# Kernel tuning notes

Hardware: AMD Instinct MI355X
Metric: run time of the kernel (lower is better)

## Reference

```python
import jax, jax.numpy as jnp
import numpy as np

N = 50000      # nodes
E = 800000     # edges (avg degree 16)
D_IN = 256
H = 128
D_OUT = 64
L = 3
EPS = 1e-5


def setup_inputs() -> dict:
    key = jax.random.key(0)
    ks = jax.random.split(key, 12)
    s = 0.05
    x = jax.random.normal(ks[0], (N, D_IN), jnp.float32)
    edge_index = jax.random.randint(ks[1], (2, E), 0, N, dtype=jnp.int32)
    edge_attr = jax.random.normal(ks[2], (E,), jnp.float32)
    # in / out projections
    W_in = jax.random.normal(ks[3], (D_IN, H), jnp.float32) * s
    b_in = jnp.zeros((H,), jnp.float32)
    W_out = jax.random.normal(ks[4], (H, D_OUT), jnp.float32) * s
    # per-layer ResGatedGraphConv params (stacked over L layers)
    Wk = jax.random.normal(ks[5], (L, H, H), jnp.float32) * s
    Wq = jax.random.normal(ks[6], (L, H, H), jnp.float32) * s
    Wv = jax.random.normal(ks[7], (L, H, H), jnp.float32) * s
    Ws = jax.random.normal(ks[8], (L, H, H), jnp.float32) * s  # lin_skip (no bias)
    We = jax.random.normal(ks[9], (L, 1, H), jnp.float32) * s  # lin_edge
    bk = jnp.zeros((L, H), jnp.float32)
    bq = jnp.zeros((L, H), jnp.float32)
    bv = jnp.zeros((L, H), jnp.float32)
    be = jnp.zeros((L, H), jnp.float32)
    b_gcn = jnp.zeros((L, H), jnp.float32)  # conv bias
    gamma = jnp.ones((L, H), jnp.float32)
    beta = jnp.zeros((L, H), jnp.float32)
    return {
        "x": x, "edge_attr": edge_attr,
        "W_in": W_in, "b_in": b_in,
        "Wk": Wk, "bk": bk, "Wq": Wq, "bq": bq, "Wv": Wv, "bv": bv,
        "We": We, "be": be, "Ws": Ws, "b_gcn": b_gcn,
        "gamma": gamma, "beta": beta, "W_out": W_out,
        "edge_index": edge_index,
    }


def _layernorm(h, g, b):
    mu = jnp.mean(h, axis=-1, keepdims=True)
    var = jnp.mean((h - mu) ** 2, axis=-1, keepdims=True)
    return (h - mu) * jax.lax.rsqrt(var + EPS) * g + b


def reference(x, edge_attr, W_in, b_in, Wk, bk, Wq, bq, Wv, bv, We, be, Ws,
              b_gcn, gamma, beta, W_out, edge_index):
    src = edge_index[0]  # x_j (source)
    dst = edge_index[1]  # x_i (target)
    ea = edge_attr[:, None]  # [E, 1]
    h = x @ W_in + b_in  # dropout_prob = 0 -> identity
    for l in range(L):
        k = h @ Wk[l] + bk[l]          # lin_key(x_i basis)  [N, H]
        q = h @ Wq[l] + bq[l]          # lin_query(x_j)      [N, H]
        v = h @ Wv[l] + bv[l]          # lin_value(x_j)      [N, H]
        e = ea @ We[l] + be[l]         # lin_edge            [E, H]
        # PyG message: sigmoid((k_i+e) + (q_j+e)) * (v_j+e)
        gate = jax.nn.sigmoid(k[dst] + q[src] + 2.0 * e)
        msg = gate * (v[src] + e)      # [E, H]
        agg = jax.ops.segment_sum(msg, dst, num_segments=N)  # add-aggregation
        h = agg + h @ Ws[l] + b_gcn[l]  # root weight + bias
        h = _layernorm(h, gamma[l], beta[l])
        h = jax.nn.gelu(h, approximate=False)  # torch nn.GELU default (erf)
    return h @ W_out  # out_proj, bias=False
```

## Files before the change

kernel.cpp:

```cpp
#include <hip/hip_runtime.h>

#define N_NODES 50000
#define NPAD    50048
#define E_EDGES 800000
#define DIN 256
#define H 128
#define DOUT 64
#define EPSF 1e-5f
#define NBLK 196
#define RT   1563
#define CVB  12500
#define PKB  928
#define HSB  3125
#define SCB  782
#define NSHARD 8
#define SHARD_SZ 100000

typedef __bf16 bf16x8 __attribute__((ext_vector_type(8)));
typedef float  f32x4  __attribute__((ext_vector_type(4)));
typedef float  f32x2  __attribute__((ext_vector_type(2)));
typedef unsigned short ushort_t;
typedef unsigned int   uint_t;

#define L2E 1.4426950408889634f
#define LN2 0.6931471805599453f

#if __has_builtin(__builtin_amdgcn_exp2f)
#define EXP2F(x) __builtin_amdgcn_exp2f(x)
#else
#define EXP2F(x) __expf((x) * LN2)
#endif

__device__ inline float bf2f(uint_t u) {
    union { uint_t i; float f; } v; v.i = u << 16; return v.f;
}
__device__ inline ushort_t f2bf(float f) {
    uint_t u = __float_as_uint(f);
    uint_t r = (u + 0x7fffu + ((u >> 16) & 1u)) >> 16;
    return (ushort_t)r;
}

#if __has_builtin(__builtin_amdgcn_cvt_f32_fp8)
#define FP8DEC(u, s) __builtin_amdgcn_cvt_f32_fp8((uint_t)(u), (s))
#else
__device__ inline float fp8_dec_sw(uint_t b) {
    uint_t s = (b & 0x80u) << 24;
    uint_t em = b & 0x7fu;
    if (em < 8u) return __uint_as_float(s);
    uint_t ex = (em >> 3) + 120u;
    uint_t mn = (em & 7u) << 20;
    return __uint_as_float(s | (ex << 23) | mn);
}
#define FP8DEC(u, s) fp8_dec_sw(((uint_t)(u) >> (8 * (s))) & 0xffu)
#endif

#if __has_builtin(__builtin_amdgcn_cvt_pk_f32_fp8)
__device__ __forceinline__ f32x2 cvtpk_q(uint_t u) {
    auto r = __builtin_amdgcn_cvt_pk_f32_fp8(u, false);
    f32x2 o; o.x = r[0]; o.y = r[1]; return o;
}
#else
__device__ __forceinline__ f32x2 cvtpk_q(uint_t u) {
    f32x2 r; r.x = FP8DEC(u, 0); r.y = FP8DEC(u, 1); return r;
}
#endif

#if __has_builtin(__builtin_amdgcn_cvt_pk_fp8_f32)
__device__ inline uint_t fp8_pk(float a, float b) {
    return (uint_t)__builtin_amdgcn_cvt_pk_fp8_f32(a, b, 0, false) & 0xffffu;
}
#else
__device__ inline uint_t fp8_enc_sw(float f) {
    uint_t u = __float_as_uint(f);
    uint_t s = (u >> 24) & 0x80u;
    uint_t a = u & 0x7fffffffu;
    if (a < 0x3c800000u) return s;
    if (a > 0x43e00000u) a = 0x43e00000u;
    uint_t r = a + 0x7ffffu + ((a >> 20) & 1u);
    uint_t ex = (r >> 23) - 120u;
    uint_t mn = (r >> 20) & 7u;
    return s | (ex << 3) | mn;
}
__device__ inline uint_t fp8_pk(float a, float b) {
    return fp8_enc_sw(a) | (fp8_enc_sw(b) << 8);
}
#endif

__global__ __launch_bounds__(256) void k_pre(const float* __restrict__ x, ushort_t* __restrict__ xb,
                                             const float* __restrict__ Wk, const float* __restrict__ Wq,
                                             const float* __restrict__ Wv, const float* __restrict__ Ws,
                                             const float* __restrict__ W_in, const float* __restrict__ W_out,
                                             ushort_t* __restrict__ Bq, ushort_t* __restrict__ Bin,
                                             ushort_t* __restrict__ Bout,
                                             const int* __restrict__ ei, int* __restrict__ deg8,
                                             int* __restrict__ rank)
{
    int b = blockIdx.x;
    int tid = threadIdx.x;
    if (b < CVB) {
        int i = b * 256 + tid;
        float4 v = ((const float4*)x)[i];
        ushort4 o;
        o.x = f2bf(v.x); o.y = f2bf(v.y); o.z = f2bf(v.z); o.w = f2bf(v.w);
        ((ushort4*)xb)[i] = o;
    } else if (b < CVB + PKB) {
        int t = (b - CVB) * 256 + tid;
        if (t < 196608) {
            int l = t >> 16;
            int r = t & 65535;
            int c = r >> 7;
            int k = r & 127;
            int m = c >> 7;
            int cm = c & 127;
            const float* W = (m == 0) ? Wk : (m == 1) ? Wq : (m == 2) ? Wv : Ws;
            Bq[t] = f2bf(W[(size_t)l * H * H + k * H + cm]);
        } else if (t < 229376) {
            int t2 = t - 196608;
            int c = t2 >> 8;
            int k = t2 & 255;
            Bin[t2] = f2bf(W_in[k * H + c]);
        } else {
            int t3 = t - 229376;
            int c = t3 >> 7;
            int k = t3 & 127;
            Bout[t3] = f2bf(W_out[k * DOUT + c]);
        }
    } else {
        int e = (b - CVB - PKB) * 256 + tid;
        int dst = ei[E_EDGES + e];
        int shard = e / SHARD_SZ;
        rank[e] = atomicAdd(&deg8[shard * N_NODES + dst], 1);
    }
}

__global__ __launch_bounds__(256) void k_mid(const ushort_t* __restrict__ xb,
                                             const ushort_t* __restrict__ Bin,
                                             const float* __restrict__ b_in,
                                             ushort_t* __restrict__ hb,
                                             const int* __restrict__ ei,
                                             const float* __restrict__ ea,
                                             const int* __restrict__ deg8,
                                             const int* __restrict__ rank,
                                             uint2* __restrict__ csr)
{
    int blk = blockIdx.x;
    int tid = threadIdx.x;
    if (blk < RT) {
        int gw = blk * 4 + (tid >> 6);
        int lane = tid & 63;
        int rt = gw >> 2, c32 = (gw & 3) * 32;
        int r0 = rt * 32;
        const ushort_t* Ap = xb + (size_t)(r0 + (lane & 15)) * DIN + 8 * (lane >> 4);
        const ushort_t* Bp = Bin + (size_t)(c32 + (lane & 15)) * DIN + 8 * (lane >> 4);
        f32x4 acc[2][2];
        #pragma unroll
        for (int rb = 0; rb < 2; ++rb)
            #pragma unroll
            for (int nf = 0; nf < 2; ++nf) acc[rb][nf] = (f32x4){0.f, 0.f, 0.f, 0.f};
        #pragma unroll
        for (int ks = 0; ks < 8; ++ks) {
            bf16x8 a0 = *(const bf16x8*)(Ap + ks * 32);
            bf16x8 a1 = *(const bf16x8*)(Ap + 16 * DIN + ks * 32);
            bf16x8 b0 = *(const bf16x8*)(Bp + ks * 32);
            bf16x8 b1 = *(const bf16x8*)(Bp + 16 * DIN + ks * 32);
            acc[0][0] = __builtin_amdgcn_mfma_f32_16x16x32_bf16(a0, b0, acc[0][0], 0, 0, 0);
            acc[1][0] = __builtin_amdgcn_mfma_f32_16x16x32_bf16(a1, b0, acc[1][0], 0, 0, 0);
            acc[0][1] = __builtin_amdgcn_mfma_f32_16x16x32_bf16(a0, b1, acc[0][1], 0, 0, 0);
            acc[1][1] = __builtin_amdgcn_mfma_f32_16x16x32_bf16(a1, b1, acc[1][1], 0, 0, 0);
        }
        int rowoff = (lane >> 4) << 2;
        #pragma unroll
        for (int nf = 0; nf < 2; ++nf) {
            int col = c32 + nf * 16 + (lane & 15);
            float bb = b_in[col];
            #pragma unroll
            for (int rb = 0; rb < 2; ++rb)
                #pragma unroll
                for (int j = 0; j < 4; ++j)
                    hb[(size_t)(r0 + rb * 16 + rowoff + j) * H + col] = f2bf(acc[rb][nf][j] + bb);
        }
    } else {
        int e0 = (blk - RT) * 1024 + tid;
        #pragma unroll
        for (int k = 0; k < 4; ++k) {
            int e = e0 + k * 256;
            if (e < E_EDGES) {
                int src = ei[e];
                int dst = ei[E_EDGES + e];
                int shard = e / SHARD_SZ;
                int pos = deg8[shard * N_NODES + dst] + rank[e];
                csr[pos] = make_uint2((uint_t)src, __float_as_uint(ea[e]));
            }
        }
    }
}

__global__ __launch_bounds__(256) void k_qkvs_mfma(const ushort_t* __restrict__ hb,
                                                   const ushort_t* __restrict__ Bq,
                                                   const float* __restrict__ bk, const float* __restrict__ bq,
                                                   const float* __restrict__ bv, const float* __restrict__ bs,
                                                   ushort_t* __restrict__ qf8, uint_t* __restrict__ vb,
                                                   uint_t* __restrict__ ks)
{
    int gw = blockIdx.x * 4 + (threadIdx.x >> 6);
    int lane = threadIdx.x & 63;
    int rt = gw >> 3, cfg = gw & 7;
    int pair = cfg >> 2, c32 = (cfg & 3) * 32;
    int r0 = rt * 32;
    const ushort_t* Ap = hb + (size_t)(r0 + (lane & 15)) * H + 8 * (lane >> 4);
    int cb0 = pair ? 0   : 128;
    int cb1 = pair ? 384 : 256;
    const ushort_t* Bp0 = Bq + (size_t)(cb0 + c32 + (lane & 15)) * H + 8 * (lane >> 4);
    const ushort_t* Bp1 = Bq + (size_t)(cb1 + c32 + (lane & 15)) * H + 8 * (lane >> 4);
    f32x4 acc[2][2][2];
    #pragma unroll
    for (int rb = 0; rb < 2; ++rb)
        #pragma unroll
        for (int m = 0; m < 2; ++m)
            #pragma unroll
            for (int nf = 0; nf < 2; ++nf) acc[rb][m][nf] = (f32x4){0.f, 0.f, 0.f, 0.f};
    #pragma unroll
    for (int kk = 0; kk < 4; ++kk) {
        bf16x8 a0 = *(const bf16x8*)(Ap + kk * 32);
        bf16x8 a1 = *(const bf16x8*)(Ap + 16 * H + kk * 32);
        #pragma unroll
        for (int nf = 0; nf < 2; ++nf) {
            bf16x8 b0 = *(const bf16x8*)(Bp0 + nf * 16 * H + kk * 32);
            bf16x8 b1 = *(const bf16x8*)(Bp1 + nf * 16 * H + kk * 32);
            acc[0][0][nf] = __builtin_amdgcn_mfma_f32_16x16x32_bf16(a0, b0, acc[0][0][nf], 0, 0, 0);
            acc[1][0][nf] = __builtin_amdgcn_mfma_f32_16x16x32_bf16(a1, b0, acc[1][0][nf], 0, 0, 0);
            acc[0][1][nf] = __builtin_amdgcn_mfma_f32_16x16x32_bf16(a0, b1, acc[0][1][nf], 0, 0, 0);
            acc[1][1][nf] = __builtin_amdgcn_mfma_f32_16x16x32_bf16(a1, b1, acc[1][1][nf], 0, 0, 0);
        }
    }
    int rowoff = (lane >> 4) << 2;
    int l15 = lane & 15;
    if (pair == 0) {
        int col_lo = c32 + l15, col_hi = col_lo + 16;
        int e = (c32 >> 1) + l15;
        float bql = bq[col_lo], bqh = bq[col_hi];
        float bvl = bv[col_lo], bvh = bv[col_hi];
        #pragma unroll
        for (int rb = 0; rb < 2; ++rb)
            #pragma unroll
            for (int j = 0; j < 4; ++j) {
                size_t row = r0 + rb * 16 + rowoff + j;
                float ql = (acc[rb][0][0][j] + bql) * L2E;
                float qh = (acc[rb][0][1][j] + bqh) * L2E;
                qf8[row * 64 + e] = (ushort_t)fp8_pk(ql, qh);
                uint_t vl = f2bf(acc[rb][1][0][j] + bvl);
                uint_t vh = f2bf(acc[rb][1][1][j] + bvh);
                vb[row * 64 + e] = (vh << 16) | vl;
            }
    } else {
        #pragma unroll
        for (int nf = 0; nf < 2; ++nf) {
            int col = c32 + nf * 16 + l15;
            float bbk = bk[col], bbs = bs[col];
            #pragma unroll
            for (int rb = 0; rb < 2; ++rb)
                #pragma unroll
                for (int j = 0; j < 4; ++j) {
                    size_t row = r0 + rb * 16 + rowoff + j;
                    uint_t kkv = f2bf((acc[rb][0][nf][j] + bbk) * L2E);
                    uint_t ssv = f2bf(acc[rb][1][nf][j] + bbs);
                    ks[row * H + col] = (ssv << 16) | kkv;
                }
        }
    }
}

__global__ __launch_bounds__(256) void k_bsum(const int* __restrict__ deg8, int* __restrict__ bsum)
{
    __shared__ int ws[4];
    int t = threadIdx.x;
    int i = blockIdx.x * 256 + t;
    int v = 0;
    if (i < N_NODES) {
        #pragma unroll
        for (int s = 0; s < NSHARD; ++s) v += deg8[s * N_NODES + i];
    }
    #pragma unroll
    for (int off = 32; off > 0; off >>= 1) v += __shfl_down(v, off);
    if ((t & 63) == 0) ws[t >> 6] = v;
    __syncthreads();
    if (t == 0) bsum[blockIdx.x] = ws[0] + ws[1] + ws[2] + ws[3];
}

__global__ __launch_bounds__(256) void k_bscan(const int* __restrict__ bsum, int* __restrict__ boff)
{
    __shared__ int ws[4];
    int t = threadIdx.x;
    int v = (t < NBLK) ? bsum[t] : 0;
    int lane = t & 63, wid = t >> 6;
    int inc = v;
    #pragma unroll
    for (int off = 1; off < 64; off <<= 1) {
        int u = __shfl_up(inc, off);
        if (lane >= off) inc += u;
    }
    if (lane == 63) ws[wid] = inc;
    __syncthreads();
    if (t == 0) {
        int s = 0;
        #pragma unroll
        for (int w = 0; w < 4; ++w) { int x = ws[w]; ws[w] = s; s += x; }
    }
    __syncthreads();
    if (t < NBLK) boff[t] = inc - v + ws[wid];
}

__global__ __launch_bounds__(256) void k_rowptr(int* __restrict__ deg8,
                                                const int* __restrict__ boff,
                                                int* __restrict__ rowptr)
{
    __shared__ int ws[4];
    int t = threadIdx.x;
    int i = blockIdx.x * 256 + t;
    int d[NSHARD];
    int v = 0;
    if (i < N_NODES) {
        #pragma unroll
        for (int s = 0; s < NSHARD; ++s) { d[s] = deg8[s * N_NODES + i]; v += d[s]; }
    }
    int lane = t & 63, wid = t >> 6;
    int inc = v;
    #pragma unroll
    for (int off = 1; off < 64; off <<= 1) {
        int u = __shfl_up(inc, off);
        if (lane >= off) inc += u;
    }
    if (lane == 63) ws[wid] = inc;
    __syncthreads();
    if (t == 0) {
        int s = 0;
        #pragma unroll
        for (int w = 0; w < 4; ++w) { int x = ws[w]; ws[w] = s; s += x; }
    }
    __syncthreads();
    int excl = inc - v + ws[wid] + boff[blockIdx.x];
    if (i < N_NODES) {
        rowptr[i] = excl;
        int run = excl;
        #pragma unroll
        for (int s = 0; s < NSHARD; ++s) { int dd = d[s]; deg8[s * N_NODES + i] = run; run += dd; }
    }
    if (i == N_NODES - 1) rowptr[N_NODES] = excl + v;
}

__device__ __forceinline__ void edge_acc(uint_t qw, uint_t uv, float ea,
                                         f32x2 we2, f32x2 be2, f32x2 kd2, f32x2& acc)
{
    f32x2 q = cvtpk_q(qw);
    f32x2 v;
    v.x = __uint_as_float(uv << 16);
    v.y = __uint_as_float(uv & 0xffff0000u);
    f32x2 av; av.x = ea; av.y = ea;
    f32x2 ep = __builtin_elementwise_fma(av, we2, be2);
    f32x2 g  = __builtin_elementwise_fma((f32x2){2.f, 2.f}, ep, kd2 + q);
    f32x2 ex; ex.x = EXP2F(-g.x); ex.y = EXP2F(-g.y);
    f32x2 d = ex + (f32x2){1.f, 1.f};
    f32x2 sg; sg.x = __builtin_amdgcn_rcpf(d.x); sg.y = __builtin_amdgcn_rcpf(d.y);
    f32x2 m = __builtin_elementwise_fma((f32x2){LN2, LN2}, ep, v);
    acc = __builtin_elementwise_fma(sg, m, acc);
}

__global__ __launch_bounds__(256) void k_agg_ln(const int* __restrict__ rowptr,
                                                const uint2* __restrict__ csr,
                                                const ushort_t* __restrict__ qf8,
                                                const uint_t* __restrict__ vb,
                                                const uint_t* __restrict__ ks,
                                                const float* __restrict__ We,
                                                const float* __restrict__ be,
                                                const float* __restrict__ gamma,
                                                const float* __restrict__ beta,
                                                ushort_t* __restrict__ hout)
{
    int tid = threadIdx.x;
    int lane = tid & 63;
    int node = __builtin_amdgcn_readfirstlane(blockIdx.x * 4 + (tid >> 6));
    int flo = ((lane >> 4) << 5) + (lane & 15);
    int fhi = flo + 16;

    f32x2 we2, be2, kd2, acc;
    we2.x = We[flo] * L2E; we2.y = We[fhi] * L2E;
    be2.x = be[flo] * L2E; be2.y = be[fhi] * L2E;
    uint_t klo = ks[(size_t)node * H + flo];
    uint_t khi = ks[(size_t)node * H + fhi];
    kd2.x = bf2f(klo & 0xffffu); kd2.y = bf2f(khi & 0xffffu);
    acc.x = bf2f(klo >> 16);     acc.y = bf2f(khi >> 16);
    int p = rowptr[node];
    int pend = rowptr[node + 1];

#define GATH(QW, UV, A, C) { \
    A = __uint_as_float((C).y); \
    const ushort_t* qrow_ = qf8 + ((size_t)(C).x << 6); \
    const uint_t*   vrow_ = vb  + ((size_t)(C).x << 6); \
    QW = qrow_[lane]; \
    UV = vrow_[lane]; }

    while (p + 8 <= pend) {
        uint2 c0 = csr[p],     c1 = csr[p + 1], c2 = csr[p + 2], c3 = csr[p + 3];
        uint2 c4 = csr[p + 4], c5 = csr[p + 5], c6 = csr[p + 6], c7 = csr[p + 7];
        uint_t w0, w1, w2, w3, w4, w5, w6, w7;
        uint_t u0, u1, u2, u3, u4, u5, u6, u7;
        float a0, a1, a2, a3, a4, a5, a6, a7;
        GATH(w0, u0, a0, c0); GATH(w1, u1, a1, c1); GATH(w2, u2, a2, c2); GATH(w3, u3, a3, c3);
        GATH(w4, u4, a4, c4); GATH(w5, u5, a5, c5); GATH(w6, u6, a6, c6); GATH(w7, u7, a7, c7);
        edge_acc(w0, u0, a0, we2, be2, kd2, acc);
        edge_acc(w1, u1, a1, we2, be2, kd2, acc);
        edge_acc(w2, u2, a2, we2, be2, kd2, acc);
        edge_acc(w3, u3, a3, we2, be2, kd2, acc);
        edge_acc(w4, u4, a4, we2, be2, kd2, acc);
        edge_acc(w5, u5, a5, we2, be2, kd2, acc);
        edge_acc(w6, u6, a6, we2, be2, kd2, acc);
        edge_acc(w7, u7, a7, we2, be2, kd2, acc);
        p += 8;
    }
    if (p + 4 <= pend) {
        uint2 c0 = csr[p], c1 = csr[p + 1], c2 = csr[p + 2], c3 = csr[p + 3];
        uint_t w0, w1, w2, w3;
        uint_t u0, u1, u2, u3;
        float a0, a1, a2, a3;
        GATH(w0, u0, a0, c0); GATH(w1, u1, a1, c1); GATH(w2, u2, a2, c2); GATH(w3, u3, a3, c3);
        edge_acc(w0, u0, a0, we2, be2, kd2, acc);
        edge_acc(w1, u1, a1, we2, be2, kd2, acc);
        edge_acc(w2, u2, a2, we2, be2, kd2, acc);
        edge_acc(w3, u3, a3, we2, be2, kd2, acc);
        p += 4;
    }
    for (; p < pend; ++p) {
        uint2 c = csr[p];
        uint_t qw, uv; float a;
        GATH(qw, uv, a, c);
        edge_acc(qw, uv, a, we2, be2, kd2, acc);
    }
#undef GATH

    float s  = acc.x + acc.y;
    float s2 = acc.x * acc.x + acc.y * acc.y;
    #pragma unroll
    for (int off = 32; off > 0; off >>= 1) {
        s  += __shfl_down(s, off);
        s2 += __shfl_down(s2, off);
    }
    s  = __shfl(s, 0);
    s2 = __shfl(s2, 0);
    float mu  = s * (1.f / H);
    float var = s2 * (1.f / H) - mu * mu;
    float rstd = rsqrtf(var + EPSF);
    float glo = gamma[flo], ghi = gamma[fhi];
    float blo = beta[flo],  bhi = beta[fhi];
    float y0 = (acc.x - mu) * rstd * glo + blo;
    float y1 = (acc.y - mu) * rstd * ghi + bhi;
    y0 = 0.5f * y0 * (1.f + erff(y0 * 0.70710678118f));
    y1 = 0.5f * y1 * (1.f + erff(y1 * 0.70710678118f));
    hout[(size_t)node * H + flo] = f2bf(y0);
    hout[(size_t)node * H + fhi] = f2bf(y1);
}

__global__ __launch_bounds__(256) void k_out_mfma(const ushort_t* __restrict__ hb,
                                                  const ushort_t* __restrict__ Bout,
                                                  float* __restrict__ out)
{
    int gw = blockIdx.x * 4 + (threadIdx.x >> 6);
    if (gw >= 6250) return;
    int lane = threadIdx.x & 63;
    int rg = gw >> 1, cg = gw & 1;
    int r0 = rg * 16, c0 = cg * 32;
    const ushort_t* Ap = hb + (size_t)(r0 + (lane & 15)) * H + 8 * (lane >> 4);
    const ushort_t* Bp = Bout + (size_t)(c0 + (lane & 15)) * H + 8 * (lane >> 4);
    f32x4 acc[2];
    acc[0] = (f32x4){0.f, 0.f, 0.f, 0.f};
    acc[1] = (f32x4){0.f, 0.f, 0.f, 0.f};
    #pragma unroll
    for (int kk = 0; kk < 4; ++kk) {
        bf16x8 a = *(const bf16x8*)(Ap + kk * 32);
        bf16x8 b0 = *(const bf16x8*)(Bp + kk * 32);
        bf16x8 b1 = *(const bf16x8*)(Bp + 16 * H + kk * 32);
        acc[0] = __builtin_amdgcn_mfma_f32_16x16x32_bf16(a, b0, acc[0], 0, 0, 0);
        acc[1] = __builtin_amdgcn_mfma_f32_16x16x32_bf16(a, b1, acc[1], 0, 0, 0);
    }
    int rowb = r0 + ((lane >> 4) << 2);
    #pragma unroll
    for (int nf = 0; nf < 2; ++nf) {
        int col = c0 + nf * 16 + (lane & 15);
        #pragma unroll
        for (int j = 0; j < 4; ++j)
            out[(size_t)(rowb + j) * DOUT + col] = acc[nf][j];
    }
}

extern "C" void kernel_launch(void* const* d_in, const int* in_sizes, int n_in,
                              void* d_out, int out_size, void* d_ws, size_t ws_size,
                              hipStream_t stream) {
    const float* x         = (const float*)d_in[0];
    const float* edge_attr = (const float*)d_in[1];
    const float* W_in      = (const float*)d_in[2];
    const float* b_in      = (const float*)d_in[3];
    const float* Wk        = (const float*)d_in[4];
    const float* bk        = (const float*)d_in[5];
    const float* Wq        = (const float*)d_in[6];
    const float* bq        = (const float*)d_in[7];
    const float* Wv        = (const float*)d_in[8];
    const float* bv        = (const float*)d_in[9];
    const float* We        = (const float*)d_in[10];
    const float* be        = (const float*)d_in[11];
    const float* Ws        = (const float*)d_in[12];
    const float* b_gcn     = (const float*)d_in[13];
    const float* gamma     = (const float*)d_in[14];
    const float* beta      = (const float*)d_in[15];
    const float* W_out     = (const float*)d_in[16];
    const int*   edge_index= (const int*)d_in[17];
    float* out = (float*)d_out;

    char* wsb = (char*)d_ws;
    ushort_t* hb  = (ushort_t*)wsb;                  wsb += (size_t)NPAD * H * 2;
    ushort_t* qf8 = (ushort_t*)wsb;                  wsb += (size_t)NPAD * 64 * 2;
    uint_t*   vb  = (uint_t*)wsb;                    wsb += (size_t)NPAD * 64 * 4;
    uint_t*   ks  = (uint_t*)wsb;                    wsb += (size_t)NPAD * H * 4;
    ushort_t* xb  = (ushort_t*)wsb;                  wsb += (size_t)NPAD * DIN * 2;
    ushort_t* Bq  = (ushort_t*)wsb;                  wsb += 3 * 512 * 128 * 2;
    ushort_t* Bin = (ushort_t*)wsb;                  wsb += 128 * 256 * 2;
    ushort_t* Bout= (ushort_t*)wsb;                  wsb += 64 * 128 * 2;
    uint2* csr    = (uint2*)wsb;                     wsb += (size_t)E_EDGES * 8;
    int*   rank   = (int*)wsb;                       wsb += (size_t)E_EDGES * 4;
    int*   deg8   = (int*)wsb;                       wsb += (size_t)NSHARD * N_NODES * 4;
    int*   rowptr = (int*)wsb;                       wsb += (N_NODES + 1) * 4;
    int*   bsum   = (int*)wsb;                       wsb += NBLK * 4;
    int*   boff   = (int*)wsb;                       wsb += NBLK * 4;

    (void)hipMemsetAsync(deg8, 0, (size_t)NSHARD * N_NODES * sizeof(int), stream);

    k_pre<<<CVB + PKB + HSB, 256, 0, stream>>>(x, xb, Wk, Wq, Wv, Ws, W_in, W_out,
                                               Bq, Bin, Bout, edge_index, deg8, rank);
    k_bsum<<<NBLK, 256, 0, stream>>>(deg8, bsum);
    k_bscan<<<1, 256, 0, stream>>>(bsum, boff);
    k_rowptr<<<NBLK, 256, 0, stream>>>(deg8, boff, rowptr);

    k_mid<<<RT + SCB, 256, 0, stream>>>(xb, Bin, b_in, hb,
                                        edge_index, edge_attr, deg8, rank, csr);

    for (int l = 0; l < 3; ++l) {
        k_qkvs_mfma<<<2 * RT, 256, 0, stream>>>(hb, Bq + (size_t)l * 512 * 128,
                                                bk + l * H, bq + l * H, bv + l * H, b_gcn + l * H,
                                                qf8, vb, ks);
        k_agg_ln<<<N_NODES / 4, 256, 0, stream>>>(rowptr, csr, qf8, vb, ks,
                                                  We + l * H, be + l * H,
                                                  gamma + l * H, beta + l * H, hb);
    }
    k_out_mfma<<<RT, 256, 0, stream>>>(hb, Bout, out);
}
```

Baseline: 374.0 us.

## Split CSR scatter across k_mid and first qkvs launch, scatter blocks first

The CSR edge scatter is split in half. The first half runs as the leading blocks of k_mid, ahead of the input-projection GEMM blocks. The second half is folded into the layer-0 k_qkvs_mfma launch as extra leading blocks, so the memory-bound scatter overlaps with MFMA GEMM work in two kernels. Loads in the scatter helper are also batched before the dependent deg8 lookups and stores to expose more memory-level parallelism. Adds kernel parameters and a branch to the qkvs kernel; correctness relies on CSR only being needed by k_agg_ln, which runs after both launches.

```diff
diff --git a/kernel.cpp b/kernel.cpp
--- a/kernel.cpp
+++ b/kernel.cpp
@@ -12,9 +12,10 @@
 #define CVB  12500
 #define PKB  928
 #define HSB  3125
-#define SCB  782
 #define NSHARD 8
 #define SHARD_SZ 100000
+#define SCHALF 391
+#define EHALF  400384
 
 typedef __bf16 bf16x8 __attribute__((ext_vector_type(8)));
 typedef float  f32x4  __attribute__((ext_vector_type(4)));
@@ -85,6 +86,33 @@
     return fp8_enc_sw(a) | (fp8_enc_sw(b) << 8);
 }
 #endif
+
+__device__ __forceinline__ void do_scatter4(int e0, const int* __restrict__ ei,
+                                            const float* __restrict__ ea,
+                                            const int* __restrict__ deg8,
+                                            const int* __restrict__ rank,
+                                            uint2* __restrict__ csr)
+{
+    int src[4], dst[4], rk[4];
+    float a[4];
+    bool ok[4];
+    #pragma unroll
+    for (int k = 0; k < 4; ++k) {
+        int e = e0 + k * 256;
+        ok[k] = e < E_EDGES;
+        if (ok[k]) { src[k] = ei[e]; dst[k] = ei[E_EDGES + e]; a[k] = ea[e]; rk[k] = rank[e]; }
+    }
+    int pos[4];
+    #pragma unroll
+    for (int k = 0; k < 4; ++k)
+        if (ok[k]) {
+            int e = e0 + k * 256;
+            pos[k] = deg8[(e / SHARD_SZ) * N_NODES + dst[k]] + rk[k];
+        }
+    #pragma unroll
+    for (int k = 0; k < 4; ++k)
+        if (ok[k]) csr[pos[k]] = make_uint2((uint_t)src[k], __float_as_uint(a[k]));
+}
 
 __global__ __launch_bounds__(256) void k_pre(const float* __restrict__ x, ushort_t* __restrict__ xb,
                                              const float* __restrict__ Wk, const float* __restrict__ Wq,
@@ -145,8 +173,10 @@
 {
     int blk = blockIdx.x;
     int tid = threadIdx.x;
-    if (blk < RT) {
-        int gw = blk * 4 + (tid >> 6);
+    if (blk < SCHALF) {
+        do_scatter4(blk * 1024 + tid, ei, ea, deg8, rank, csr);
+    } else {
+        int gw = (blk - SCHALF) * 4 + (tid >> 6);
         int lane = tid & 63;
         int rt = gw >> 2, c32 = (gw & 3) * 32;
         int r0 = rt * 32;
@@ -179,19 +209,6 @@
                 for (int j = 0; j < 4; ++j)
                     hb[(size_t)(r0 + rb * 16 + rowoff + j) * H + col] = f2bf(acc[rb][nf][j] + bb);
         }
-    } else {
-        int e0 = (blk - RT) * 1024 + tid;
-        #pragma unroll
-        for (int k = 0; k < 4; ++k) {
-            int e = e0 + k * 256;
-            if (e < E_EDGES) {
-                int src = ei[e];
-                int dst = ei[E_EDGES + e];
-                int shard = e / SHARD_SZ;
-                int pos = deg8[shard * N_NODES + dst] + rank[e];
-                csr[pos] = make_uint2((uint_t)src, __float_as_uint(ea[e]));
-            }
-        }
     }
 }
 
@@ -200,10 +217,22 @@
                                                    const float* __restrict__ bk, const float* __restrict__ bq,
                                                    const float* __restrict__ bv, const float* __restrict__ bs,
                                                    ushort_t* __restrict__ qf8, uint_t* __restrict__ vb,
-                                                   uint_t* __restrict__ ks)
-{
-    int gw = blockIdx.x * 4 + (threadIdx.x >> 6);
-    int lane = threadIdx.x & 63;
+                                                   uint_t* __restrict__ ks,
+                                                   const int* __restrict__ ei,
+                                                   const float* __restrict__ ea,
+                                                   const int* __restrict__ deg8,
+                                                   const int* __restrict__ rank,
+                                                   uint2* __restrict__ csr,
+                                                   int scount, int sbase)
+{
+    int blk = blockIdx.x;
+    int tid = threadIdx.x;
+    if (blk < scount) {
+        do_scatter4(sbase + blk * 1024 + tid, ei, ea, deg8, rank, csr);
+        return;
+    }
+    int gw = (blk - scount) * 4 + (tid >> 6);
+    int lane = tid & 63;
     int rt = gw >> 3, cfg = gw & 7;
     int pair = cfg >> 2, c32 = (cfg & 3) * 32;
     int r0 = rt * 32;
@@ -538,13 +567,16 @@
     k_bscan<<<1, 256, 0, stream>>>(bsum, boff);
     k_rowptr<<<NBLK, 256, 0, stream>>>(deg8, boff, rowptr);
 
-    k_mid<<<RT + SCB, 256, 0, stream>>>(xb, Bin, b_in, hb,
-                                        edge_index, edge_attr, deg8, rank, csr);
+    k_mid<<<SCHALF + RT, 256, 0, stream>>>(xb, Bin, b_in, hb,
+                                           edge_index, edge_attr, deg8, rank, csr);
 
     for (int l = 0; l < 3; ++l) {
-        k_qkvs_mfma<<<2 * RT, 256, 0, stream>>>(hb, Bq + (size_t)l * 512 * 128,
+        int scount = (l == 0) ? SCHALF : 0;
+        k_qkvs_mfma<<<scount + 2 * RT, 256, 0, stream>>>(hb, Bq + (size_t)l * 512 * 128,
                                                 bk + l * H, bq + l * H, bv + l * H, b_gcn + l * H,
-                                                qf8, vb, ks);
+                                                qf8, vb, ks,
+                                                edge_index, edge_attr, deg8, rank, csr,
+                                                scount, EHALF);
         k_agg_ln<<<N_NODES / 4, 256, 0, stream>>>(rowptr, csr, qf8, vb, ks,
                                                   We + l * H, be + l * H,
                                                   gamma + l * H, beta + l * H, hb);
```

Measured after the change: 371.1 us. About the same (-0.8%).
